# Optimization experiments

Hardware: AMD Instinct MI355X
Metric: run time of the kernel (lower is better)

## Reference

```python
import jax, jax.numpy as jnp
import numpy as np

INPUT_DIM, HIDDEN, LATENT, HEADS = 4, 32, 2, 4
N_NODES, N_EDGES = 50000, 800000
EPS_BN = 1e-5
NEG_SLOPE = 0.2


def _glorot(key, shape):
    fan_in, fan_out = shape[0], shape[-1]
    lim = jnp.sqrt(6.0 / (fan_in + fan_out))
    return jax.random.uniform(key, shape, jnp.float32, -lim, lim)


def setup_inputs() -> dict:
    key = jax.random.key(0)
    ks = jax.random.split(key, 20)
    x = jax.random.normal(ks[0], (N_NODES, INPUT_DIM), jnp.float32)
    edge_index = jax.random.randint(ks[1], (2, N_EDGES), 0, N_NODES, jnp.int64)

    def gat_params(k, in_ch, out_ch, heads, concat):
        k1, k2, k3 = jax.random.split(k, 3)
        W = _glorot(k1, (in_ch, heads * out_ch))
        a_src = _glorot(k2, (heads, out_ch))
        a_dst = _glorot(k3, (heads, out_ch))
        b = jnp.zeros((heads * out_ch,) if concat else (out_ch,), jnp.float32)
        return W, a_src, a_dst, b

    w_e1, as_e1, ad_e1, b_e1 = gat_params(ks[2], INPUT_DIM, HIDDEN, HEADS, True)
    w_e3, as_e3, ad_e3, b_e3 = gat_params(ks[3], HIDDEN * HEADS, LATENT, 1, False)
    w_d1, as_d1, ad_d1, b_d1 = gat_params(ks[4], LATENT, HIDDEN, HEADS, True)
    w_d3, as_d3, ad_d3, b_d3 = gat_params(ks[5], HIDDEN * HEADS, INPUT_DIM, 1, False)

    return dict(
        x=x, edge_index=edge_index,
        bn_gamma=jnp.ones((INPUT_DIM,), jnp.float32),
        bn_beta=jnp.zeros((INPUT_DIM,), jnp.float32),
        w_e1=w_e1, as_e1=as_e1, ad_e1=ad_e1, b_e1=b_e1,
        w_e3=w_e3, as_e3=as_e3, ad_e3=ad_e3, b_e3=b_e3,
        w_d1=w_d1, as_d1=as_d1, ad_d1=ad_d1, b_d1=b_d1,
        w_d3=w_d3, as_d3=as_d3, ad_d3=ad_d3, b_d3=b_d3,
    )


def gat_conv(x, src, dst, W, a_src, a_dst, b, heads, out_ch, concat):
    """PyG-style GATConv: gather -> attention -> segment softmax -> scatter."""
    n = x.shape[0]
    h = (x @ W).reshape(n, heads, out_ch)                 # [N,H,C]
    alpha_s = jnp.sum(h * a_src, axis=-1)                 # [N,H]
    alpha_d = jnp.sum(h * a_dst, axis=-1)                 # [N,H]
    e = jax.nn.leaky_relu(alpha_s[src] + alpha_d[dst], NEG_SLOPE)  # [E,H]
    # numerically-stable softmax over incoming edges of each dst node
    m = jax.ops.segment_max(e, dst, num_segments=n)
    e = jnp.exp(e - m[dst])
    s = jax.ops.segment_sum(e, dst, num_segments=n)
    a = e / (s[dst] + 1e-16)                              # [E,H]
    msg = h[src] * a[:, :, None]                          # [E,H,C]
    out = jax.ops.segment_sum(msg, dst, num_segments=n)   # [N,H,C]
    out = out.reshape(n, heads * out_ch) if concat else out.mean(axis=1)
    return out + b


def reference(x, edge_index, bn_gamma, bn_beta,
              w_e1, as_e1, ad_e1, b_e1,
              w_e3, as_e3, ad_e3, b_e3,
              w_d1, as_d1, ad_d1, b_d1,
              w_d3, as_d3, ad_d3, b_d3):
    n = x.shape[0]
    # GATConv default add_self_loops=True
    loops = jnp.arange(n, dtype=edge_index.dtype)
    src = jnp.concatenate([edge_index[0], loops])
    dst = jnp.concatenate([edge_index[1], loops])

    # BatchNorm1d (training-mode batch statistics, biased variance)
    mu = x.mean(axis=0)
    var = x.var(axis=0)
    x_in = (x - mu) * jax.lax.rsqrt(var + EPS_BN) * bn_gamma + bn_beta

    enc1 = jax.nn.relu(gat_conv(x_in, src, dst, w_e1, as_e1, ad_e1, b_e1, HEADS, HIDDEN, True))
    latent = gat_conv(enc1, src, dst, w_e3, as_e3, ad_e3, b_e3, 1, LATENT, False)
    dec1 = jax.nn.relu(gat_conv(latent, src, dst, w_d1, as_d1, ad_d1, b_d1, HEADS, HIDDEN, True))
    x_out = gat_conv(dec1, src, dst, w_d3, as_d3, ad_d3, b_d3, 1, INPUT_DIM, False)
    return x_out
```

## Files before the change

kernel.cpp:

```cpp
#include <hip/hip_runtime.h>

#define NN 50000
#define E0 800000
#define ET 850000
#define EPS_BN 1e-5f
#define SLOPE 0.2f
#define NBP 32
#define EPC 8192
#define NCH 104
#define PBITS 9
#define NP 98
#define SCN (NP*NCH)

__device__ __forceinline__ float lrelu(float v){ return v > 0.f ? v : SLOPE*v; }

__global__ __launch_bounds__(1024) void chunk_hist_bn(const int* __restrict__ ei, int* __restrict__ chunkcnt,
                                                      const float* __restrict__ x, float* __restrict__ part){
  __shared__ int cc[NP];
  int t = threadIdx.x;
  for (int i=t; i<NP; i+=1024) cc[i]=0;
  __syncthreads();
  int base = blockIdx.x*EPC;
  int end = min(base+EPC, ET);
  for (int e = base+t; e < end; e += 1024){
    int dst = (e < E0) ? ei[E0 + e] : (e - E0);
    atomicAdd(&cc[dst>>PBITS], 1);
  }
  __syncthreads();
  for (int i=t; i<NP; i+=1024) chunkcnt[blockIdx.x*NP + i] = cc[i];

  if (blockIdx.x < NBP){
    float s[4]={0,0,0,0}, q[4]={0,0,0,0};
    for (int n = blockIdx.x*1024 + t; n < NN; n += NBP*1024){
      float4 v = reinterpret_cast<const float4*>(x)[n];
      s[0]+=v.x; s[1]+=v.y; s[2]+=v.z; s[3]+=v.w;
      q[0]+=v.x*v.x; q[1]+=v.y*v.y; q[2]+=v.z*v.z; q[3]+=v.w*v.w;
    }
    #pragma unroll
    for (int m=1;m<64;m<<=1){
      #pragma unroll
      for (int i=0;i<4;i++){ s[i]+=__shfl_xor(s[i],m); q[i]+=__shfl_xor(q[i],m); }
    }
    __shared__ float lds[16][8];
    int wid = t>>6, lane = t&63;
    if (lane==0){
      #pragma unroll
      for (int i=0;i<4;i++){ lds[wid][i]=s[i]; lds[wid][4+i]=q[i]; }
    }
    __syncthreads();
    if (t < 8){
      float p = 0.f;
      #pragma unroll
      for (int w=0;w<16;w++) p += lds[w][t];
      part[blockIdx.x*8 + t] = p;
    }
  }
}

__global__ __launch_bounds__(1024) void scan_fold(
    const int* __restrict__ chunkcnt, int* __restrict__ pofs,
    const float* __restrict__ part, const float* __restrict__ gamma, const float* __restrict__ beta,
    const float* __restrict__ w_e1, const float* __restrict__ as_e1, const float* __restrict__ ad_e1,
    const float* __restrict__ w_d1, const float* __restrict__ as_d1, const float* __restrict__ ad_d1,
    float* __restrict__ sclsft, float* __restrict__ fold){
  __shared__ int wsum[1024];
  int t = threadIdx.x;
  const int PER = (SCN + 1023)/1024;
  int vals[PER];
  int mysum = 0;
  #pragma unroll
  for (int k=0;k<PER;k++){
    int idx = t*PER + k;
    int v = 0;
    if (idx < SCN){ int p = idx/NCH, ch = idx - p*NCH; v = chunkcnt[ch*NP + p]; }
    vals[k] = v; mysum += v;
  }
  wsum[t] = mysum; __syncthreads();
  int val = mysum;
  for (int off=1; off<1024; off<<=1){
    int tmp = (t>=off) ? wsum[t-off] : 0;
    __syncthreads();
    val += tmp; wsum[t] = val; __syncthreads();
  }
  int run = val - mysum;
  #pragma unroll
  for (int k=0;k<PER;k++){
    int idx = t*PER + k;
    if (idx < SCN){ int p = idx/NCH, ch = idx - p*NCH; pofs[ch*NP + p] = run; }
    run += vals[k];
  }

  if (t < 64){
    int ch = t&7, bslot = t>>3;
    float s = 0.f;
    for (int b=bslot; b<NBP; b+=8) s += part[b*8 + ch];
    s += __shfl_xor(s,8); s += __shfl_xor(s,16); s += __shfl_xor(s,32);
    float qv = __shfl(s, (t&3)+4);
    if (t < 4){
      float mu  = s*(1.0f/NN);
      float var = qv*(1.0f/NN) - mu*mu;
      float scl = rsqrtf(var + EPS_BN)*gamma[t];
      sclsft[t]   = scl;
      sclsft[4+t] = beta[t] - mu*scl;
    }
  } else if (t < 128){
    int u = t - 64;
    if (u < 32){
      int idx = u & 15; int h = idx>>2; int i = idx&3;
      const float* a = (u<16) ? as_e1 : ad_e1;
      float sum = 0.f;
      for (int c=0;c<32;c++) sum += w_e1[i*128 + h*32 + c] * a[h*32 + c];
      fold[u] = sum;
    } else if (u < 48){
      int idx = u - 32; int j = idx & 7; int h = j>>1; int i = j&1;
      const float* a = (idx<8) ? as_d1 : ad_d1;
      float sum = 0.f;
      for (int c=0;c<32;c++) sum += w_d1[i*128 + h*32 + c] * a[h*32 + c];
      fold[32 + idx] = sum;
    }
  }
}

__global__ __launch_bounds__(1024) void partition_pass(const int* __restrict__ ei,
                                                       const int* __restrict__ pofs,
                                                       int2* __restrict__ pedge){
  __shared__ int cur[NP];
  int t = threadIdx.x;
  for (int i=t; i<NP; i+=1024) cur[i] = pofs[blockIdx.x*NP + i];
  __syncthreads();
  int base = blockIdx.x*EPC;
  int end = min(base+EPC, ET);
  for (int e = base+t; e < end; e += 1024){
    int src, dst;
    if (e < E0){ src = ei[e]; dst = ei[E0+e]; } else { src = dst = e - E0; }
    int pos = atomicAdd(&cur[dst>>PBITS], 1);
    pedge[pos] = make_int2(src, dst);
  }
}

__global__ __launch_bounds__(1024) void fine_build(const int2* __restrict__ pedge,
                                                   const int* __restrict__ pofs,
                                                   int* __restrict__ rowptr, int* __restrict__ ssrc){
  int p = blockIdx.x;
  int pstart = pofs[p];
  int pend = (p+1 < NP) ? pofs[p+1] : ET;
  int dbase = p << PBITS;
  __shared__ int hist[1<<PBITS];
  __shared__ int cur[1<<PBITS];
  int t = threadIdx.x;
  if (t < 512) hist[t] = 0;
  __syncthreads();
  for (int i = pstart + t; i < pend; i += 1024)
    atomicAdd(&hist[pedge[i].y - dbase], 1);
  __syncthreads();
  int orig = (t < 512) ? hist[t] : 0;
  __syncthreads();
  int v = orig;
  for (int off=1; off<512; off<<=1){
    int tmp = (t>=off && t<512) ? hist[t-off] : 0;
    __syncthreads();
    if (t < 512){ v += tmp; hist[t] = v; }
    __syncthreads();
  }
  if (t < 512){
    int excl = v - orig;
    int d = dbase + t;
    if (d < NN) rowptr[d] = pstart + excl;
    if (p == NP-1 && t == 0) rowptr[NN] = ET;
    cur[t] = pstart + excl;
  }
  __syncthreads();
  for (int i = pstart + t; i < pend; i += 1024){
    int2 e = pedge[i];
    int pos = atomicAdd(&cur[e.y - dbase], 1);
    ssrc[pos] = e.x;
  }
}

__global__ __launch_bounds__(256) void eagg1(
    const float* __restrict__ x, const float* __restrict__ sclsft, const float* __restrict__ fold,
    const int* __restrict__ rowptr, const int* __restrict__ ssrc,
    const float* __restrict__ w_e1, const float* __restrict__ b_e1, const float* __restrict__ w_e3,
    float2* __restrict__ pk2){
  int dst = blockIdx.x*64 + (threadIdx.x>>2);
  int sub = threadIdx.x & 3;
  if (dst >= NN) return;
  float sc[8];
  #pragma unroll
  for (int i=0;i<8;i++) sc[i] = sclsft[i];
  float fs[16];
  #pragma unroll
  for (int i=0;i<16;i++) fs[i] = fold[i];
  float4 xd = reinterpret_cast<const float4*>(x)[dst];
  float xbd[4] = {xd.x*sc[0]+sc[4], xd.y*sc[1]+sc[5], xd.z*sc[2]+sc[6], xd.w*sc[3]+sc[7]};
  float ald[4];
  #pragma unroll
  for (int h=0;h<4;h++)
    ald[h] = xbd[0]*fold[16+h*4+0] + xbd[1]*fold[16+h*4+1]
           + xbd[2]*fold[16+h*4+2] + xbd[3]*fold[16+h*4+3];
  int r0 = rowptr[dst], r1 = rowptr[dst+1];
  float sum[4] = {0,0,0,0};
  float acc[4][4] = {{0,0,0,0},{0,0,0,0},{0,0,0,0},{0,0,0,0}};
  for (int i = r0 + sub; i < r1; i += 4){
    int s = ssrc[i];
    float4 xs = reinterpret_cast<const float4*>(x)[s];
    float xb[4] = {xs.x*sc[0]+sc[4], xs.y*sc[1]+sc[5], xs.z*sc[2]+sc[6], xs.w*sc[3]+sc[7]};
    #pragma unroll
    for (int h=0;h<4;h++){
      float a = xb[0]*fs[h*4+0] + xb[1]*fs[h*4+1] + xb[2]*fs[h*4+2] + xb[3]*fs[h*4+3];
      float w = __expf(lrelu(a + ald[h]));
      sum[h] += w;
      acc[h][0] += w*xb[0]; acc[h][1] += w*xb[1]; acc[h][2] += w*xb[2]; acc[h][3] += w*xb[3];
    }
  }
  #pragma unroll
  for (int m=1;m<4;m<<=1){
    #pragma unroll
    for (int h=0;h<4;h++){
      sum[h] += __shfl_xor(sum[h],m);
      #pragma unroll
      for (int c=0;c<4;c++) acc[h][c] += __shfl_xor(acc[h][c],m);
    }
  }
  float G0=acc[0][0], G1=acc[0][1], G2=acc[0][2], G3=acc[0][3], GS=sum[0];
  #pragma unroll
  for (int h=1;h<4;h++){
    if (sub==h){ G0=acc[h][0]; G1=acc[h][1]; G2=acc[h][2]; G3=acc[h][3]; GS=sum[h]; }
  }
  float inv = 1.f/(GS+1e-16f);
  G0*=inv; G1*=inv; G2*=inv; G3*=inv;
  float p0 = 0.f, p1 = 0.f;
  int ob = sub*32;
  #pragma unroll
  for (int q=0;q<8;q++){
    int o = ob + q*4;
    float4 b  = *reinterpret_cast<const float4*>(b_e1 + o);
    float4 w0 = *reinterpret_cast<const float4*>(w_e1 + 0*128 + o);
    float4 w1 = *reinterpret_cast<const float4*>(w_e1 + 1*128 + o);
    float4 w2 = *reinterpret_cast<const float4*>(w_e1 + 2*128 + o);
    float4 w3 = *reinterpret_cast<const float4*>(w_e1 + 3*128 + o);
    float e0 = fmaxf(b.x + G0*w0.x + G1*w1.x + G2*w2.x + G3*w3.x, 0.f);
    float e1 = fmaxf(b.y + G0*w0.y + G1*w1.y + G2*w2.y + G3*w3.y, 0.f);
    float e2 = fmaxf(b.z + G0*w0.z + G1*w1.z + G2*w2.z + G3*w3.z, 0.f);
    float e3 = fmaxf(b.w + G0*w0.w + G1*w1.w + G2*w2.w + G3*w3.w, 0.f);
    float4 wa = *reinterpret_cast<const float4*>(w_e3 + o*2);
    float4 wb = *reinterpret_cast<const float4*>(w_e3 + o*2 + 4);
    p0 += e0*wa.x + e1*wa.z + e2*wb.x + e3*wb.z;
    p1 += e0*wa.y + e1*wa.w + e2*wb.y + e3*wb.w;
  }
  p0 += __shfl_xor(p0,1); p0 += __shfl_xor(p0,2);
  p1 += __shfl_xor(p1,1); p1 += __shfl_xor(p1,2);
  if (sub==0) pk2[dst] = make_float2(p0, p1);
}

__global__ __launch_bounds__(256) void eagg2(
    const float2* __restrict__ pk2,
    const int* __restrict__ rowptr, const int* __restrict__ ssrc,
    const float* __restrict__ as_e3, const float* __restrict__ ad_e3, const float* __restrict__ b_e3,
    float2* __restrict__ lat2){
  int dst = blockIdx.x*64 + (threadIdx.x>>2);
  int sub = threadIdx.x & 3;
  if (dst >= NN) return;
  float as0 = as_e3[0], as1 = as_e3[1];
  float2 pd = pk2[dst];
  float adv = pd.x*ad_e3[0] + pd.y*ad_e3[1];
  int r0 = rowptr[dst], r1 = rowptr[dst+1];
  float sum = 0.f, a0 = 0.f, a1 = 0.f;
  for (int i = r0 + sub; i < r1; i += 4){
    int s = ssrc[i];
    float2 p = pk2[s];
    float w = __expf(lrelu(p.x*as0 + p.y*as1 + adv));
    sum += w; a0 += w*p.x; a1 += w*p.y;
  }
  #pragma unroll
  for (int m=1;m<4;m<<=1){
    sum += __shfl_xor(sum,m); a0 += __shfl_xor(a0,m); a1 += __shfl_xor(a1,m);
  }
  if (sub==0){
    float inv = 1.f/(sum+1e-16f);
    lat2[dst] = make_float2(a0*inv + b_e3[0], a1*inv + b_e3[1]);
  }
}

__global__ __launch_bounds__(256) void eagg3(
    const float2* __restrict__ lat2, const float* __restrict__ fold,
    const int* __restrict__ rowptr, const int* __restrict__ ssrc,
    const float* __restrict__ w_d1, const float* __restrict__ b_d1, const float* __restrict__ w_d3,
    float4* __restrict__ pk4){
  int dst = blockIdx.x*64 + (threadIdx.x>>2);
  int sub = threadIdx.x & 3;
  if (dst >= NN) return;
  float f3[8];
  #pragma unroll
  for (int i=0;i<8;i++) f3[i] = fold[32+i];
  float2 ld = lat2[dst];
  float ald[4];
  #pragma unroll
  for (int h=0;h<4;h++) ald[h] = ld.x*fold[40+h*2+0] + ld.y*fold[40+h*2+1];
  int r0 = rowptr[dst], r1 = rowptr[dst+1];
  float sum[4] = {0,0,0,0};
  float acc[4][2] = {{0,0},{0,0},{0,0},{0,0}};
  for (int i = r0 + sub; i < r1; i += 4){
    int s = ssrc[i];
    float2 l = lat2[s];
    #pragma unroll
    for (int h=0;h<4;h++){
      float a = l.x*f3[h*2+0] + l.y*f3[h*2+1];
      float w = __expf(lrelu(a + ald[h]));
      sum[h] += w;
      acc[h][0] += w*l.x; acc[h][1] += w*l.y;
    }
  }
  #pragma unroll
  for (int m=1;m<4;m<<=1){
    #pragma unroll
    for (int h=0;h<4;h++){
      sum[h] += __shfl_xor(sum[h],m);
      acc[h][0] += __shfl_xor(acc[h][0],m);
      acc[h][1] += __shfl_xor(acc[h][1],m);
    }
  }
  float G0=acc[0][0], G1=acc[0][1], GS=sum[0];
  #pragma unroll
  for (int h=1;h<4;h++){
    if (sub==h){ G0=acc[h][0]; G1=acc[h][1]; GS=sum[h]; }
  }
  float inv = 1.f/(GS+1e-16f);
  G0*=inv; G1*=inv;
  float p0=0.f,p1=0.f,p2=0.f,p3=0.f;
  int ob = sub*32;
  #pragma unroll
  for (int q=0;q<8;q++){
    int o = ob + q*4;
    float4 b  = *reinterpret_cast<const float4*>(b_d1 + o);
    float4 w0 = *reinterpret_cast<const float4*>(w_d1 + 0*128 + o);
    float4 w1 = *reinterpret_cast<const float4*>(w_d1 + 1*128 + o);
    float e0 = fmaxf(b.x + G0*w0.x + G1*w1.x, 0.f);
    float e1 = fmaxf(b.y + G0*w0.y + G1*w1.y, 0.f);
    float e2 = fmaxf(b.z + G0*w0.z + G1*w1.z, 0.f);
    float e3 = fmaxf(b.w + G0*w0.w + G1*w1.w, 0.f);
    float4 d0 = *reinterpret_cast<const float4*>(w_d3 + (o+0)*4);
    float4 d1 = *reinterpret_cast<const float4*>(w_d3 + (o+1)*4);
    float4 d2 = *reinterpret_cast<const float4*>(w_d3 + (o+2)*4);
    float4 d3v= *reinterpret_cast<const float4*>(w_d3 + (o+3)*4);
    p0 += e0*d0.x + e1*d1.x + e2*d2.x + e3*d3v.x;
    p1 += e0*d0.y + e1*d1.y + e2*d2.y + e3*d3v.y;
    p2 += e0*d0.z + e1*d1.z + e2*d2.z + e3*d3v.z;
    p3 += e0*d0.w + e1*d1.w + e2*d2.w + e3*d3v.w;
  }
  #pragma unroll
  for (int m=1;m<4;m<<=1){
    p0 += __shfl_xor(p0,m); p1 += __shfl_xor(p1,m);
    p2 += __shfl_xor(p2,m); p3 += __shfl_xor(p3,m);
  }
  if (sub==0) pk4[dst] = make_float4(p0,p1,p2,p3);
}

__global__ __launch_bounds__(256) void eagg4(
    const float4* __restrict__ pk4,
    const int* __restrict__ rowptr, const int* __restrict__ ssrc,
    const float* __restrict__ as_d3, const float* __restrict__ ad_d3, const float* __restrict__ b_d3,
    float* __restrict__ out){
  int dst = blockIdx.x*64 + (threadIdx.x>>2);
  int sub = threadIdx.x & 3;
  if (dst >= NN) return;
  float as0=as_d3[0], as1=as_d3[1], as2=as_d3[2], as3=as_d3[3];
  float4 hd = pk4[dst];
  float adv = hd.x*ad_d3[0] + hd.y*ad_d3[1] + hd.z*ad_d3[2] + hd.w*ad_d3[3];
  int r0 = rowptr[dst], r1 = rowptr[dst+1];
  float sum = 0.f, a0=0.f, a1=0.f, a2=0.f, a3=0.f;
  for (int i = r0 + sub; i < r1; i += 4){
    int s = ssrc[i];
    float4 f = pk4[s];
    float w = __expf(lrelu(f.x*as0 + f.y*as1 + f.z*as2 + f.w*as3 + adv));
    sum += w; a0 += w*f.x; a1 += w*f.y; a2 += w*f.z; a3 += w*f.w;
  }
  #pragma unroll
  for (int m=1;m<4;m<<=1){
    sum += __shfl_xor(sum,m);
    a0 += __shfl_xor(a0,m); a1 += __shfl_xor(a1,m);
    a2 += __shfl_xor(a2,m); a3 += __shfl_xor(a3,m);
  }
  if (sub==0){
    float inv = 1.f/(sum+1e-16f);
    reinterpret_cast<float4*>(out)[dst] =
      make_float4(a0*inv+b_d3[0], a1*inv+b_d3[1], a2*inv+b_d3[2], a3*inv+b_d3[3]);
  }
}

extern "C" void kernel_launch(void* const* d_in, const int* in_sizes, int n_in,
                              void* d_out, int out_size, void* d_ws, size_t ws_size,
                              hipStream_t stream) {
  const float* x     = (const float*)d_in[0];
  const int*   ei    = (const int*)  d_in[1];
  const float* gamma = (const float*)d_in[2];
  const float* beta  = (const float*)d_in[3];
  const float* w_e1  = (const float*)d_in[4];
  const float* as_e1 = (const float*)d_in[5];
  const float* ad_e1 = (const float*)d_in[6];
  const float* b_e1  = (const float*)d_in[7];
  const float* w_e3  = (const float*)d_in[8];
  const float* as_e3 = (const float*)d_in[9];
  const float* ad_e3 = (const float*)d_in[10];
  const float* b_e3  = (const float*)d_in[11];
  const float* w_d1  = (const float*)d_in[12];
  const float* as_d1 = (const float*)d_in[13];
  const float* ad_d1 = (const float*)d_in[14];
  const float* b_d1  = (const float*)d_in[15];
  const float* w_d3  = (const float*)d_in[16];
  const float* as_d3 = (const float*)d_in[17];
  const float* ad_d3 = (const float*)d_in[18];
  const float* b_d3  = (const float*)d_in[19];

  char* ws = (char*)d_ws;
  size_t off = 0;
  auto alloc = [&](size_t bytes)->void*{
    void* p = ws + off;
    off += (bytes + 255) & ~(size_t)255;
    return p;
  };
  int*    chunkcnt = (int*)   alloc((size_t)SCN*4);
  int*    pofs     = (int*)   alloc((size_t)SCN*4);
  int2*   pedge    = (int2*)  alloc((size_t)ET*8);
  int*    rowptr   = (int*)   alloc((size_t)(NN+1)*4);
  int*    ssrc     = (int*)   alloc((size_t)ET*4);
  float*  part     = (float*) alloc((size_t)NBP*8*4);
  float*  sclsft   = (float*) alloc(32);
  float*  fold     = (float*) alloc(64*4);
  float2* pk2      = (float2*)alloc((size_t)NN*8);
  float2* lat2     = (float2*)alloc((size_t)NN*8);
  float4* pk4      = (float4*)alloc((size_t)NN*16);

  chunk_hist_bn<<<NCH, 1024, 0, stream>>>(ei, chunkcnt, x, part);
  scan_fold<<<1, 1024, 0, stream>>>(chunkcnt, pofs, part, gamma, beta,
                                    w_e1, as_e1, ad_e1, w_d1, as_d1, ad_d1, sclsft, fold);
  partition_pass<<<NCH, 1024, 0, stream>>>(ei, pofs, pedge);
  fine_build<<<NP, 1024, 0, stream>>>(pedge, pofs, rowptr, ssrc);

  const int NAGG = (NN + 63)/64;

  eagg1<<<NAGG, 256, 0, stream>>>(x, sclsft, fold, rowptr, ssrc, w_e1, b_e1, w_e3, pk2);
  eagg2<<<NAGG, 256, 0, stream>>>(pk2, rowptr, ssrc, as_e3, ad_e3, b_e3, lat2);
  eagg3<<<NAGG, 256, 0, stream>>>(lat2, fold, rowptr, ssrc, w_d1, b_d1, w_d3, pk4);
  eagg4<<<NAGG, 256, 0, stream>>>(pk4, rowptr, ssrc, as_d3, ad_d3, b_d3, (float*)d_out);
}
```

Measured before the change: 124.1 us.

## Fold scan into histogram kernel, pack edges, and store sources as 16-bit

The separate scan/fold kernel is merged into the histogram kernel. The last block to finish, found through an atomic counter, does the prefix scan, the BatchNorm statistics and the weight folding. Partitioned edges are packed into one 32-bit word (src plus low dst bits), and the CSR source array becomes unsigned short, cutting traffic in the build and in all four aggregation kernels. Partitions shrink to 256 nodes with smaller edge chunks, which makes the single-block scan about eight times larger and relies on the counter starting at a multiple of the block count.

```diff
diff --git a/kernel.cpp b/kernel.cpp
--- a/kernel.cpp
+++ b/kernel.cpp
@@ -6,32 +6,42 @@
 #define EPS_BN 1e-5f
 #define SLOPE 0.2f
 #define NBP 32
-#define EPC 8192
-#define NCH 104
-#define PBITS 9
-#define NP 98
+#define EPC 2048
+#define NCH 416
+#define PBITS 8
+#define PSZ 256
+#define NP 196
 #define SCN (NP*NCH)
+#define PER 80
 
 __device__ __forceinline__ float lrelu(float v){ return v > 0.f ? v : SLOPE*v; }
 
-__global__ __launch_bounds__(1024) void chunk_hist_bn(const int* __restrict__ ei, int* __restrict__ chunkcnt,
-                                                      const float* __restrict__ x, float* __restrict__ part){
+__global__ __launch_bounds__(1024) void k1_hist_bn_scan(
+    const int* __restrict__ ei, const float* __restrict__ x,
+    int* __restrict__ chunkcnt, float* __restrict__ part, unsigned* __restrict__ counter,
+    const float* __restrict__ gamma, const float* __restrict__ beta,
+    const float* __restrict__ w_e1, const float* __restrict__ as_e1, const float* __restrict__ ad_e1,
+    const float* __restrict__ w_d1, const float* __restrict__ as_d1, const float* __restrict__ ad_d1,
+    int* __restrict__ pofs, float* __restrict__ sclsft, float* __restrict__ fold){
   __shared__ int cc[NP];
-  int t = threadIdx.x;
-  for (int i=t; i<NP; i+=1024) cc[i]=0;
-  __syncthreads();
-  int base = blockIdx.x*EPC;
-  int end = min(base+EPC, ET);
-  for (int e = base+t; e < end; e += 1024){
-    int dst = (e < E0) ? ei[E0 + e] : (e - E0);
-    atomicAdd(&cc[dst>>PBITS], 1);
-  }
-  __syncthreads();
-  for (int i=t; i<NP; i+=1024) chunkcnt[blockIdx.x*NP + i] = cc[i];
-
-  if (blockIdx.x < NBP){
+  __shared__ float bnlds[16][8];
+  __shared__ int sh[1024];
+  __shared__ int lastf;
+  const int b = blockIdx.x, t = threadIdx.x;
+
+  for (int i=t;i<NP;i+=1024) cc[i]=0;
+  __syncthreads();
+  int base=b*EPC, end=min(base+EPC,ET);
+  for (int e=base+t; e<end; e+=1024){
+    int dst = (e<E0) ? ei[E0+e] : (e-E0);
+    atomicAdd(&cc[dst>>PBITS],1);
+  }
+  __syncthreads();
+  for (int i=t;i<NP;i+=1024) chunkcnt[b*NP+i]=cc[i];
+
+  if (b < NBP){
     float s[4]={0,0,0,0}, q[4]={0,0,0,0};
-    for (int n = blockIdx.x*1024 + t; n < NN; n += NBP*1024){
+    for (int n=b*1024+t; n<NN; n+=NBP*1024){
       float4 v = reinterpret_cast<const float4*>(x)[n];
       s[0]+=v.x; s[1]+=v.y; s[2]+=v.z; s[3]+=v.w;
       q[0]+=v.x*v.x; q[1]+=v.y*v.y; q[2]+=v.z*v.z; q[3]+=v.w*v.w;
@@ -41,145 +51,139 @@
       #pragma unroll
       for (int i=0;i<4;i++){ s[i]+=__shfl_xor(s[i],m); q[i]+=__shfl_xor(q[i],m); }
     }
-    __shared__ float lds[16][8];
-    int wid = t>>6, lane = t&63;
+    int wid=t>>6, lane=t&63;
     if (lane==0){
       #pragma unroll
-      for (int i=0;i<4;i++){ lds[wid][i]=s[i]; lds[wid][4+i]=q[i]; }
+      for (int i=0;i<4;i++){ bnlds[wid][i]=s[i]; bnlds[wid][4+i]=q[i]; }
     }
     __syncthreads();
-    if (t < 8){
-      float p = 0.f;
+    if (t<8){
+      float p=0.f;
       #pragma unroll
-      for (int w=0;w<16;w++) p += lds[w][t];
-      part[blockIdx.x*8 + t] = p;
-    }
-  }
-}
-
-__global__ __launch_bounds__(1024) void scan_fold(
-    const int* __restrict__ chunkcnt, int* __restrict__ pofs,
-    const float* __restrict__ part, const float* __restrict__ gamma, const float* __restrict__ beta,
-    const float* __restrict__ w_e1, const float* __restrict__ as_e1, const float* __restrict__ ad_e1,
-    const float* __restrict__ w_d1, const float* __restrict__ as_d1, const float* __restrict__ ad_d1,
-    float* __restrict__ sclsft, float* __restrict__ fold){
-  __shared__ int wsum[1024];
-  int t = threadIdx.x;
-  const int PER = (SCN + 1023)/1024;
-  int vals[PER];
-  int mysum = 0;
-  #pragma unroll
+      for (int w=0;w<16;w++) p += bnlds[w][t];
+      part[b*8+t]=p;
+    }
+  }
+
+  __threadfence();
+  if (t==0){
+    unsigned old = atomicAdd(counter, 1u);
+    lastf = (((old+1u) % (unsigned)NCH) == 0u);
+  }
+  __syncthreads();
+  if (!lastf) return;
+  __threadfence();
+
+  int mysum=0;
   for (int k=0;k<PER;k++){
-    int idx = t*PER + k;
-    int v = 0;
-    if (idx < SCN){ int p = idx/NCH, ch = idx - p*NCH; v = chunkcnt[ch*NP + p]; }
-    vals[k] = v; mysum += v;
-  }
-  wsum[t] = mysum; __syncthreads();
-  int val = mysum;
-  for (int off=1; off<1024; off<<=1){
-    int tmp = (t>=off) ? wsum[t-off] : 0;
-    __syncthreads();
-    val += tmp; wsum[t] = val; __syncthreads();
-  }
-  int run = val - mysum;
-  #pragma unroll
+    int idx=t*PER+k;
+    if (idx<SCN){ int p=idx/NCH, ch=idx-p*NCH; mysum += chunkcnt[ch*NP+p]; }
+  }
+  sh[t]=mysum; __syncthreads();
+  int val=mysum;
+  for (int off=1;off<1024;off<<=1){
+    int tmp=(t>=off)? sh[t-off] : 0; __syncthreads();
+    val+=tmp; sh[t]=val; __syncthreads();
+  }
+  int run=val-mysum;
   for (int k=0;k<PER;k++){
-    int idx = t*PER + k;
-    if (idx < SCN){ int p = idx/NCH, ch = idx - p*NCH; pofs[ch*NP + p] = run; }
-    run += vals[k];
-  }
-
-  if (t < 64){
-    int ch = t&7, bslot = t>>3;
-    float s = 0.f;
-    for (int b=bslot; b<NBP; b+=8) s += part[b*8 + ch];
+    int idx=t*PER+k;
+    if (idx<SCN){
+      int p=idx/NCH, ch=idx-p*NCH;
+      int v=chunkcnt[ch*NP+p];
+      pofs[ch*NP+p]=run;
+      run+=v;
+    }
+  }
+
+  if (t<64){
+    int ch=t&7, bslot=t>>3;
+    float s=0.f;
+    for (int bb=bslot; bb<NBP; bb+=8) s += part[bb*8+ch];
     s += __shfl_xor(s,8); s += __shfl_xor(s,16); s += __shfl_xor(s,32);
-    float qv = __shfl(s, (t&3)+4);
-    if (t < 4){
+    float qv = __shfl(s,(t&3)+4);
+    if (t<4){
       float mu  = s*(1.0f/NN);
       float var = qv*(1.0f/NN) - mu*mu;
       float scl = rsqrtf(var + EPS_BN)*gamma[t];
       sclsft[t]   = scl;
       sclsft[4+t] = beta[t] - mu*scl;
     }
-  } else if (t < 128){
-    int u = t - 64;
-    if (u < 32){
-      int idx = u & 15; int h = idx>>2; int i = idx&3;
+  } else if (t<128){
+    int u=t-64;
+    if (u<32){
+      int idx=u&15; int h=idx>>2; int i=idx&3;
       const float* a = (u<16) ? as_e1 : ad_e1;
-      float sum = 0.f;
-      for (int c=0;c<32;c++) sum += w_e1[i*128 + h*32 + c] * a[h*32 + c];
-      fold[u] = sum;
-    } else if (u < 48){
-      int idx = u - 32; int j = idx & 7; int h = j>>1; int i = j&1;
+      float sum=0.f;
+      for (int c=0;c<32;c++) sum += w_e1[i*128+h*32+c]*a[h*32+c];
+      fold[u]=sum;
+    } else if (u<48){
+      int idx=u-32; int j=idx&7; int h=j>>1; int i=j&1;
       const float* a = (idx<8) ? as_d1 : ad_d1;
-      float sum = 0.f;
-      for (int c=0;c<32;c++) sum += w_d1[i*128 + h*32 + c] * a[h*32 + c];
-      fold[32 + idx] = sum;
-    }
-  }
-}
-
-__global__ __launch_bounds__(1024) void partition_pass(const int* __restrict__ ei,
-                                                       const int* __restrict__ pofs,
-                                                       int2* __restrict__ pedge){
+      float sum=0.f;
+      for (int c=0;c<32;c++) sum += w_d1[i*128+h*32+c]*a[h*32+c];
+      fold[32+idx]=sum;
+    }
+  }
+}
+
+__global__ __launch_bounds__(256) void partition_pass(const int* __restrict__ ei,
+                                                      const int* __restrict__ pofs,
+                                                      unsigned* __restrict__ pedge){
   __shared__ int cur[NP];
-  int t = threadIdx.x;
-  for (int i=t; i<NP; i+=1024) cur[i] = pofs[blockIdx.x*NP + i];
-  __syncthreads();
-  int base = blockIdx.x*EPC;
-  int end = min(base+EPC, ET);
-  for (int e = base+t; e < end; e += 1024){
-    int src, dst;
-    if (e < E0){ src = ei[e]; dst = ei[E0+e]; } else { src = dst = e - E0; }
-    int pos = atomicAdd(&cur[dst>>PBITS], 1);
-    pedge[pos] = make_int2(src, dst);
-  }
-}
-
-__global__ __launch_bounds__(1024) void fine_build(const int2* __restrict__ pedge,
+  const int b=blockIdx.x, t=threadIdx.x;
+  for (int i=t;i<NP;i+=256) cur[i]=pofs[b*NP+i];
+  __syncthreads();
+  int base=b*EPC, end=min(base+EPC,ET);
+  for (int e=base+t; e<end; e+=256){
+    int src,dst;
+    if (e<E0){ src=ei[e]; dst=ei[E0+e]; } else { src=dst=e-E0; }
+    int pos=atomicAdd(&cur[dst>>PBITS],1);
+    pedge[pos] = ((unsigned)src<<PBITS) | (unsigned)(dst&(PSZ-1));
+  }
+}
+
+__global__ __launch_bounds__(1024) void fine_build(const unsigned* __restrict__ pedge,
                                                    const int* __restrict__ pofs,
-                                                   int* __restrict__ rowptr, int* __restrict__ ssrc){
-  int p = blockIdx.x;
-  int pstart = pofs[p];
-  int pend = (p+1 < NP) ? pofs[p+1] : ET;
-  int dbase = p << PBITS;
-  __shared__ int hist[1<<PBITS];
-  __shared__ int cur[1<<PBITS];
-  int t = threadIdx.x;
-  if (t < 512) hist[t] = 0;
-  __syncthreads();
-  for (int i = pstart + t; i < pend; i += 1024)
-    atomicAdd(&hist[pedge[i].y - dbase], 1);
-  __syncthreads();
-  int orig = (t < 512) ? hist[t] : 0;
-  __syncthreads();
-  int v = orig;
-  for (int off=1; off<512; off<<=1){
-    int tmp = (t>=off && t<512) ? hist[t-off] : 0;
+                                                   int* __restrict__ rowptr,
+                                                   unsigned short* __restrict__ ssrc){
+  const int p=blockIdx.x, t=threadIdx.x;
+  int pstart=pofs[p];
+  int pend=(p+1<NP)? pofs[p+1] : ET;
+  int dbase=p<<PBITS;
+  __shared__ int hist[PSZ];
+  __shared__ int cur[PSZ];
+  if (t<PSZ) hist[t]=0;
+  __syncthreads();
+  for (int i=pstart+t;i<pend;i+=1024) atomicAdd(&hist[pedge[i]&(PSZ-1)],1);
+  __syncthreads();
+  int o=(t<PSZ)? hist[t] : 0;
+  __syncthreads();
+  int v=o;
+  for (int off=1;off<PSZ;off<<=1){
+    int tmp=(t>=off && t<PSZ)? hist[t-off] : 0;
     __syncthreads();
-    if (t < 512){ v += tmp; hist[t] = v; }
+    if (t<PSZ){ v+=tmp; hist[t]=v; }
     __syncthreads();
   }
-  if (t < 512){
-    int excl = v - orig;
-    int d = dbase + t;
-    if (d < NN) rowptr[d] = pstart + excl;
-    if (p == NP-1 && t == 0) rowptr[NN] = ET;
-    cur[t] = pstart + excl;
-  }
-  __syncthreads();
-  for (int i = pstart + t; i < pend; i += 1024){
-    int2 e = pedge[i];
-    int pos = atomicAdd(&cur[e.y - dbase], 1);
-    ssrc[pos] = e.x;
+  if (t<PSZ){
+    int excl=v-o;
+    int d=dbase+t;
+    if (d<NN) rowptr[d]=pstart+excl;
+    cur[t]=pstart+excl;
+  }
+  if (p==NP-1 && t==0) rowptr[NN]=ET;
+  __syncthreads();
+  for (int i=pstart+t;i<pend;i+=1024){
+    unsigned e=pedge[i];
+    int pos=atomicAdd(&cur[e&(PSZ-1)],1);
+    ssrc[pos]=(unsigned short)(e>>PBITS);
   }
 }
 
 __global__ __launch_bounds__(256) void eagg1(
     const float* __restrict__ x, const float* __restrict__ sclsft, const float* __restrict__ fold,
-    const int* __restrict__ rowptr, const int* __restrict__ ssrc,
+    const int* __restrict__ rowptr, const unsigned short* __restrict__ ssrc,
     const float* __restrict__ w_e1, const float* __restrict__ b_e1, const float* __restrict__ w_e3,
     float2* __restrict__ pk2){
   int dst = blockIdx.x*64 + (threadIdx.x>>2);
@@ -255,7 +259,7 @@
 
 __global__ __launch_bounds__(256) void eagg2(
     const float2* __restrict__ pk2,
-    const int* __restrict__ rowptr, const int* __restrict__ ssrc,
+    const int* __restrict__ rowptr, const unsigned short* __restrict__ ssrc,
     const float* __restrict__ as_e3, const float* __restrict__ ad_e3, const float* __restrict__ b_e3,
     float2* __restrict__ lat2){
   int dst = blockIdx.x*64 + (threadIdx.x>>2);
@@ -284,7 +288,7 @@
 
 __global__ __launch_bounds__(256) void eagg3(
     const float2* __restrict__ lat2, const float* __restrict__ fold,
-    const int* __restrict__ rowptr, const int* __restrict__ ssrc,
+    const int* __restrict__ rowptr, const unsigned short* __restrict__ ssrc,
     const float* __restrict__ w_d1, const float* __restrict__ b_d1, const float* __restrict__ w_d3,
     float4* __restrict__ pk4){
   int dst = blockIdx.x*64 + (threadIdx.x>>2);
@@ -358,7 +362,7 @@
 
 __global__ __launch_bounds__(256) void eagg4(
     const float4* __restrict__ pk4,
-    const int* __restrict__ rowptr, const int* __restrict__ ssrc,
+    const int* __restrict__ rowptr, const unsigned short* __restrict__ ssrc,
     const float* __restrict__ as_d3, const float* __restrict__ ad_d3, const float* __restrict__ b_d3,
     float* __restrict__ out){
   int dst = blockIdx.x*64 + (threadIdx.x>>2);
@@ -419,22 +423,23 @@
     off += (bytes + 255) & ~(size_t)255;
     return p;
   };
-  int*    chunkcnt = (int*)   alloc((size_t)SCN*4);
-  int*    pofs     = (int*)   alloc((size_t)SCN*4);
-  int2*   pedge    = (int2*)  alloc((size_t)ET*8);
-  int*    rowptr   = (int*)   alloc((size_t)(NN+1)*4);
-  int*    ssrc     = (int*)   alloc((size_t)ET*4);
-  float*  part     = (float*) alloc((size_t)NBP*8*4);
-  float*  sclsft   = (float*) alloc(32);
-  float*  fold     = (float*) alloc(64*4);
-  float2* pk2      = (float2*)alloc((size_t)NN*8);
-  float2* lat2     = (float2*)alloc((size_t)NN*8);
-  float4* pk4      = (float4*)alloc((size_t)NN*16);
-
-  chunk_hist_bn<<<NCH, 1024, 0, stream>>>(ei, chunkcnt, x, part);
-  scan_fold<<<1, 1024, 0, stream>>>(chunkcnt, pofs, part, gamma, beta,
-                                    w_e1, as_e1, ad_e1, w_d1, as_d1, ad_d1, sclsft, fold);
-  partition_pass<<<NCH, 1024, 0, stream>>>(ei, pofs, pedge);
+  int*      chunkcnt = (int*)           alloc((size_t)SCN*4);
+  int*      pofs     = (int*)           alloc((size_t)SCN*4);
+  unsigned* pedge    = (unsigned*)      alloc((size_t)ET*4);
+  int*      rowptr   = (int*)           alloc((size_t)(NN+1)*4);
+  unsigned short* ssrc = (unsigned short*)alloc((size_t)ET*2);
+  float*    part     = (float*)         alloc((size_t)NBP*8*4);
+  float*    sclsft   = (float*)         alloc(32);
+  float*    fold     = (float*)         alloc(64*4);
+  unsigned* counter  = (unsigned*)      alloc(4);
+  float2*   pk2      = (float2*)        alloc((size_t)NN*8);
+  float2*   lat2     = (float2*)        alloc((size_t)NN*8);
+  float4*   pk4      = (float4*)        alloc((size_t)NN*16);
+
+  k1_hist_bn_scan<<<NCH, 1024, 0, stream>>>(ei, x, chunkcnt, part, counter,
+                                            gamma, beta, w_e1, as_e1, ad_e1,
+                                            w_d1, as_d1, ad_d1, pofs, sclsft, fold);
+  partition_pass<<<NCH, 256, 0, stream>>>(ei, pofs, pedge);
   fine_build<<<NP, 1024, 0, stream>>>(pedge, pofs, rowptr, ssrc);
 
   const int NAGG = (NN + 63)/64;
```

Result: slower. 290.9 us (+134.3%).
